# Performance work log

Measured on AMD Instinct MI355X. Metric: run time of the kernel, lower is better.

## Reference

```python
import jax, jax.numpy as jnp
import numpy as np

LOG2 = float(np.log(2.0))


def setup_inputs() -> dict:
    key = jax.random.key(0)
    ks = jax.random.split(key, 10)
    V, G, F, T = 262144, 4096, 256, 2
    node_feats = jax.random.normal(ks[0], (V, F), dtype=jnp.float32)
    segment_ids = jnp.sort(jax.random.randint(ks[1], (V,), 0, G))
    s = 0.05
    return {
        "node_feats": node_feats,
        "segment_ids": segment_ids,
        "num_graphs": G,
        "logit_w": jax.random.normal(ks[2], (T, 2 * F, 1), dtype=jnp.float32) * s,
        "logit_b": jnp.zeros((T, 1), dtype=jnp.float32),
        "proj_w": jax.random.normal(ks[3], (T, F, F), dtype=jnp.float32) * s,
        "proj_b": jnp.zeros((T, F), dtype=jnp.float32),
        "gru_w_ih": jax.random.normal(ks[4], (T, 3 * F, F), dtype=jnp.float32) * s,
        "gru_w_hh": jax.random.normal(ks[5], (T, 3 * F, F), dtype=jnp.float32) * s,
        "gru_b_ih": jnp.zeros((T, 3 * F), dtype=jnp.float32),
        "gru_b_hh": jnp.zeros((T, 3 * F), dtype=jnp.float32),
    }


def _gru_cell(x, h, w_ih, w_hh, b_ih, b_hh):
    # torch.nn.GRUCell math
    gi = x @ w_ih.T + b_ih  # [G, 3F]
    gh = h @ w_hh.T + b_hh
    i_r, i_z, i_n = jnp.split(gi, 3, axis=-1)
    h_r, h_z, h_n = jnp.split(gh, 3, axis=-1)
    r = jax.nn.sigmoid(i_r + h_r)
    z = jax.nn.sigmoid(i_z + h_z)
    n = jnp.tanh(i_n + r * h_n)
    return (1.0 - z) * n + z * h


def reference(node_feats, segment_ids, num_graphs, logit_w, logit_b,
              proj_w, proj_b, gru_w_ih, gru_w_hh, gru_b_ih, gru_b_hh):
    G = int(num_graphs)
    # initial graph feats: sum of node feats per graph
    g_feats = jax.ops.segment_sum(node_feats, segment_ids, num_segments=G)
    T = logit_w.shape[0]
    for t in range(T):
        # broadcast relu(g_feats) to nodes, concat with node feats, compute logits
        ctx_nodes = jax.nn.relu(g_feats)[segment_ids]              # [V, F]
        z = jnp.concatenate([ctx_nodes, node_feats], axis=-1) @ logit_w[t] + logit_b[t]  # [V,1]
        z = jnp.logaddexp(z, 0.0) - LOG2                           # SoftPlus2
        # segment softmax over nodes within each graph
        zmax = jax.ops.segment_max(z, segment_ids, num_segments=G)
        e = jnp.exp(z - zmax[segment_ids])
        denom = jax.ops.segment_sum(e, segment_ids, num_segments=G)
        a = e / denom[segment_ids]                                 # [V,1]
        # project nodes (dropout=0) and attention-weighted sum per graph
        hv = node_feats @ proj_w[t] + proj_b[t]                    # [V, F]
        g_repr = jax.ops.segment_sum(a * hv, segment_ids, num_segments=G)
        context = jax.nn.elu(g_repr)
        g_feats = _gru_cell(context, g_feats, gru_w_ih[t], gru_w_hh[t], gru_b_ih[t], gru_b_hh[t])
    return g_feats
```

## Files before the change

### kernel.cpp

```cpp
#include <hip/hip_runtime.h>
#include <hip/hip_bf16.h>
#include <math.h>

#define V_NODES 262144
#define NGRAPH  4096
#define FD      256
#define TSTEPS  2
#define GP      16
#define SB      1024
#define RS      264
#define EWCAP   2560

typedef unsigned short u16;
typedef __attribute__((ext_vector_type(8))) short short8;
typedef __attribute__((ext_vector_type(4))) float f32x4;

__device__ __forceinline__ float bf2f(u16 u) {
  union { unsigned int i; float f; } x; x.i = ((unsigned int)u) << 16; return x.f;
}
__device__ __forceinline__ u16 f2bf(float f) {
  union { unsigned int i; float f; } x; x.f = f;
  unsigned int r = x.i + 0x7FFFu + ((x.i >> 16) & 1u);
  return (u16)(r >> 16);
}
__device__ __forceinline__ unsigned int pkbf(float a, float b) {
  return (unsigned int)f2bf(a) | ((unsigned int)f2bf(b) << 16);
}
__device__ __forceinline__ float softplus2(float x) {
  return fmaxf(x, 0.0f) + log1pf(__expf(-fabsf(x))) - 0.69314718056f;
}
__device__ __forceinline__ float dot8(const float4 x0, const float4 x1, const float* w) {
  float d = fmaf(x0.x, w[0], fmaf(x0.y, w[1], fmaf(x0.z, w[2], x0.w * w[3])));
  return fmaf(x1.x, w[4], fmaf(x1.y, w[5], fmaf(x1.z, w[6], fmaf(x1.w, w[7], d))));
}

__global__ __launch_bounds__(256) void k_prep(
    const int* __restrict__ seg, const float* __restrict__ w_ih,
    const float* __restrict__ w_hh, const float* __restrict__ proj_w,
    int* __restrict__ start, u16* __restrict__ wihbf, u16* __restrict__ whhbf,
    u16* __restrict__ whhlo, u16* __restrict__ pwtbf) {
  __shared__ float tl[32][33];
  const int b = blockIdx.x, tid = threadIdx.x;
  const int gtid = b * 256 + tid;
  {
    const int v = gtid;
    const int s = seg[v];
    if (v == 0) {
      for (int g = 0; g <= s; ++g) start[g] = 0;
    } else {
      const int p = seg[v - 1];
      for (int g = p + 1; g <= s; ++g) start[g] = v;
    }
    if (v == V_NODES - 1)
      for (int g = s + 1; g <= NGRAPH; ++g) start[g] = V_NODES;
  }
  {
    const int nchunk = TSTEPS * 768 * FD / 4;
    if (gtid < nchunk) {
      const float4 x = ((const float4*)w_ih)[gtid];
      uint2 u; u.x = pkbf(x.x, x.y); u.y = pkbf(x.z, x.w);
      ((uint2*)wihbf)[gtid] = u;
      const float4 y = ((const float4*)w_hh)[gtid];
      const u16 h0 = f2bf(y.x), h1 = f2bf(y.y), h2 = f2bf(y.z), h3 = f2bf(y.w);
      uint2 hi_, lo_;
      hi_.x = (unsigned)h0 | ((unsigned)h1 << 16);
      hi_.y = (unsigned)h2 | ((unsigned)h3 << 16);
      lo_.x = pkbf(y.x - bf2f(h0), y.y - bf2f(h1));
      lo_.y = pkbf(y.z - bf2f(h2), y.w - bf2f(h3));
      ((uint2*)whhbf)[gtid] = hi_;
      ((uint2*)whhlo)[gtid] = lo_;
    }
  }
  if (b < 2 * 64) {
    const int t = b >> 6, tile = b & 63, bx = tile & 7, by = tile >> 3;
    const int tx = tid & 31, ty = tid >> 5;
    const float* S = proj_w + (size_t)t * FD * FD;
    u16* D = pwtbf + (size_t)t * FD * FD;
#pragma unroll
    for (int i = 0; i < 32; i += 8)
      tl[ty + i][tx] = S[(size_t)(by * 32 + ty + i) * FD + bx * 32 + tx];
    __syncthreads();
#pragma unroll
    for (int i = 0; i < 32; i += 8)
      D[(size_t)(bx * 32 + ty + i) * FD + by * 32 + tx] = f2bf(tl[tx][ty + i]);
  }
}

__global__ __launch_bounds__(256) void k_pass1(
    const float* __restrict__ nf, const int* __restrict__ start,
    const float* __restrict__ logit_w, float* __restrict__ gf,
    u16* __restrict__ nbf, float* __restrict__ d0, float* __restrict__ d1) {
  __shared__ __align__(16) float redf[8][FD];
  const int g = blockIdx.x, tid = threadIdx.x;
  const int h = tid >> 5, sl = tid & 31;
  const int s = start[g], e = start[g + 1];
  float wA[8], wB[8];
  {
    const float4 a0 = ((const float4*)(logit_w + FD))[2 * sl];
    const float4 a1 = ((const float4*)(logit_w + FD))[2 * sl + 1];
    const float4 b0 = ((const float4*)(logit_w + 512 + FD))[2 * sl];
    const float4 b1 = ((const float4*)(logit_w + 512 + FD))[2 * sl + 1];
    wA[0]=a0.x; wA[1]=a0.y; wA[2]=a0.z; wA[3]=a0.w;
    wA[4]=a1.x; wA[5]=a1.y; wA[6]=a1.z; wA[7]=a1.w;
    wB[0]=b0.x; wB[1]=b0.y; wB[2]=b0.z; wB[3]=b0.w;
    wB[4]=b1.x; wB[5]=b1.y; wB[6]=b1.z; wB[7]=b1.w;
  }
  float ac[8];
#pragma unroll
  for (int j = 0; j < 8; ++j) ac[j] = 0.f;
  const float4* nfv = (const float4*)nf;
  int v = s + h;
  for (; v + 24 < e; v += 32) {
    float4 x0[4], x1[4];
#pragma unroll
    for (int r = 0; r < 4; ++r) {
      x0[r] = nfv[(size_t)(v + 8 * r) * 64 + 2 * sl];
      x1[r] = nfv[(size_t)(v + 8 * r) * 64 + 2 * sl + 1];
    }
#pragma unroll
    for (int r = 0; r < 4; ++r) {
      uint4 u;
      u.x = pkbf(x0[r].x, x0[r].y); u.y = pkbf(x0[r].z, x0[r].w);
      u.z = pkbf(x1[r].x, x1[r].y); u.w = pkbf(x1[r].z, x1[r].w);
      ((uint4*)(nbf + (size_t)(v + 8 * r) * FD))[sl] = u;
      ac[0] += x0[r].x; ac[1] += x0[r].y; ac[2] += x0[r].z; ac[3] += x0[r].w;
      ac[4] += x1[r].x; ac[5] += x1[r].y; ac[6] += x1[r].z; ac[7] += x1[r].w;
    }
    float dA[4], dB[4];
#pragma unroll
    for (int r = 0; r < 4; ++r) {
      dA[r] = dot8(x0[r], x1[r], wA);
      dB[r] = dot8(x0[r], x1[r], wB);
    }
#pragma unroll
    for (int off = 1; off < 32; off <<= 1) {
#pragma unroll
      for (int r = 0; r < 4; ++r) {
        dA[r] += __shfl_xor(dA[r], off, 64);
        dB[r] += __shfl_xor(dB[r], off, 64);
      }
    }
    if (sl == 0) {
#pragma unroll
      for (int r = 0; r < 4; ++r) { d0[v + 8 * r] = dA[r]; d1[v + 8 * r] = dB[r]; }
    }
  }
  for (; v < e; v += 8) {
    const float4 x0 = nfv[(size_t)v * 64 + 2 * sl];
    const float4 x1 = nfv[(size_t)v * 64 + 2 * sl + 1];
    uint4 u0;
    u0.x = pkbf(x0.x, x0.y); u0.y = pkbf(x0.z, x0.w);
    u0.z = pkbf(x1.x, x1.y); u0.w = pkbf(x1.z, x1.w);
    ((uint4*)(nbf + (size_t)v * FD))[sl] = u0;
    ac[0] += x0.x; ac[1] += x0.y; ac[2] += x0.z; ac[3] += x0.w;
    ac[4] += x1.x; ac[5] += x1.y; ac[6] += x1.z; ac[7] += x1.w;
    float dA0 = dot8(x0, x1, wA), dB0 = dot8(x0, x1, wB);
#pragma unroll
    for (int off = 1; off < 32; off <<= 1) {
      dA0 += __shfl_xor(dA0, off, 64); dB0 += __shfl_xor(dB0, off, 64);
    }
    if (sl == 0) { d0[v] = dA0; d1[v] = dB0; }
  }
  ((float4*)&redf[h][sl * 8])[0] = make_float4(ac[0], ac[1], ac[2], ac[3]);
  ((float4*)&redf[h][sl * 8])[1] = make_float4(ac[4], ac[5], ac[6], ac[7]);
  __syncthreads();
  float sum = 0.f;
#pragma unroll
  for (int j = 0; j < 8; ++j) sum += redf[j][tid];
  gf[(size_t)g * FD + tid] = sum;
}

__global__ __launch_bounds__(SB, 4) void k_steps(
    const int* __restrict__ start, const float* __restrict__ logit_w,
    const float* __restrict__ logit_b, const float* __restrict__ proj_b,
    const float* __restrict__ b_ih, const float* __restrict__ b_hh,
    const u16* __restrict__ nbf, const float* __restrict__ d0,
    const float* __restrict__ d1, float* __restrict__ gf_out,
    const u16* __restrict__ wihbf, const u16* __restrict__ whhbf,
    const u16* __restrict__ whhlo, const u16* __restrict__ pwtbf) {
  __shared__ __align__(16) float gf_s[GP][FD];
  __shared__ __align__(16) float ew[EWCAP];
  __shared__ __align__(16) u16 wns_s[GP * RS];
  __shared__ __align__(16) u16 ctx_s[GP * RS];
  __shared__ __align__(16) u16 hhi_s[GP * RS];
  __shared__ __align__(16) u16 hlo_s[GP * RS];

  const int b = blockIdx.x, tid = threadIdx.x;
  const int wv = tid >> 6, lane = tid & 63;
  const int half = lane >> 5, sl = lane & 31;
  const int g0 = b * GP;
  const int g = g0 + wv;
  const int vs = start[g0];
  const int s = start[g], e = start[g + 1];

  ((float4*)gf_s)[tid] = ((const float4*)(gf_out + (size_t)g0 * FD))[tid];
  __syncthreads();

  for (int t = 0; t < TSTEPS; ++t) {
    for (int i = tid; i < GP * FD; i += SB) {
      const float x = gf_s[i >> 8][i & 255];
      const u16 hb = f2bf(x);
      hhi_s[(i >> 8) * RS + (i & 255)] = hb;
      hlo_s[(i >> 8) * RS + (i & 255)] = f2bf(x - bf2f(hb));
    }
    {
      const float lb = logit_b[t];
      const float* dt = t ? d1 : d0;
      const float4 h4 = ((const float4*)&gf_s[wv][0])[lane];
      const float4 w4 = ((const float4*)(logit_w + (size_t)t * 512))[lane];
      float c = fmaf(fmaxf(h4.x, 0.f), w4.x, fmaf(fmaxf(h4.y, 0.f), w4.y,
                fmaf(fmaxf(h4.z, 0.f), w4.z, fmaxf(h4.w, 0.f) * w4.w)));
#pragma unroll
      for (int off = 1; off < 64; off <<= 1) c += __shfl_xor(c, off, 64);
      float m = -1e30f;
      for (int v2 = s + lane; v2 < e; v2 += 64) {
        const float z = softplus2(c + dt[v2] + lb);
        ew[v2 - vs] = z;
        m = fmaxf(m, z);
      }
#pragma unroll
      for (int off = 1; off < 64; off <<= 1) m = fmaxf(m, __shfl_xor(m, off, 64));
      float ls = 0.f;
      for (int v2 = s + lane; v2 < e; v2 += 64) {
        const float ez = __expf(ew[v2 - vs] - m);
        ew[v2 - vs] = ez;
        ls += ez;
      }
#pragma unroll
      for (int off = 1; off < 64; off <<= 1) ls += __shfl_xor(ls, off, 64);
      const float inv = (e > s) ? 1.0f / ls : 0.f;
      for (int v2 = s + lane; v2 < e; v2 += 64) ew[v2 - vs] *= inv;
      float acc[8];
#pragma unroll
      for (int j = 0; j < 8; ++j) acc[j] = 0.f;
      int v = s + half;
      for (; v + 14 < e; v += 16) {
        uint4 u[8];
#pragma unroll
        for (int r = 0; r < 8; ++r)
          u[r] = ((const uint4*)(nbf + (size_t)(v + 2 * r) * FD))[sl];
#pragma unroll
        for (int r = 0; r < 8; ++r) {
          const float a = ew[v + 2 * r - vs];
          acc[0] = fmaf(a, bf2f((u16)(u[r].x & 0xffff)), acc[0]);
          acc[1] = fmaf(a, bf2f((u16)(u[r].x >> 16)),    acc[1]);
          acc[2] = fmaf(a, bf2f((u16)(u[r].y & 0xffff)), acc[2]);
          acc[3] = fmaf(a, bf2f((u16)(u[r].y >> 16)),    acc[3]);
          acc[4] = fmaf(a, bf2f((u16)(u[r].z & 0xffff)), acc[4]);
          acc[5] = fmaf(a, bf2f((u16)(u[r].z >> 16)),    acc[5]);
          acc[6] = fmaf(a, bf2f((u16)(u[r].w & 0xffff)), acc[6]);
          acc[7] = fmaf(a, bf2f((u16)(u[r].w >> 16)),    acc[7]);
        }
      }
      for (; v < e; v += 2) {
        const uint4 u0 = ((const uint4*)(nbf + (size_t)v * FD))[sl];
        const float a0 = ew[v - vs];
        acc[0] = fmaf(a0, bf2f((u16)(u0.x & 0xffff)), acc[0]);
        acc[1] = fmaf(a0, bf2f((u16)(u0.x >> 16)),    acc[1]);
        acc[2] = fmaf(a0, bf2f((u16)(u0.y & 0xffff)), acc[2]);
        acc[3] = fmaf(a0, bf2f((u16)(u0.y >> 16)),    acc[3]);
        acc[4] = fmaf(a0, bf2f((u16)(u0.z & 0xffff)), acc[4]);
        acc[5] = fmaf(a0, bf2f((u16)(u0.z >> 16)),    acc[5]);
        acc[6] = fmaf(a0, bf2f((u16)(u0.w & 0xffff)), acc[6]);
        acc[7] = fmaf(a0, bf2f((u16)(u0.w >> 16)),    acc[7]);
      }
#pragma unroll
      for (int j = 0; j < 8; ++j) acc[j] += __shfl_xor(acc[j], 32, 64);
      if (half == 0) {
        uint4 w;
        w.x = pkbf(acc[0], acc[1]); w.y = pkbf(acc[2], acc[3]);
        w.z = pkbf(acc[4], acc[5]); w.w = pkbf(acc[6], acc[7]);
        *(uint4*)(wns_s + wv * RS + sl * 8) = w;
      }
    }
    __syncthreads();
    {
      const int r = lane & 15, q = lane >> 4;
      const u16* xp = wns_s + r * RS + q * 8;
      const u16* wp = pwtbf + (size_t)t * FD * FD + (size_t)(wv * 16 + r) * FD + q * 8;
      f32x4 a4 = {0.f, 0.f, 0.f, 0.f};
#pragma unroll
      for (int kt = 0; kt < 8; ++kt) {
        const short8 av = *(const short8*)(xp + kt * 32);
        const short8 bv = *(const short8*)(wp + kt * 32);
        a4 = __builtin_amdgcn_mfma_f32_16x16x32_bf16(av, bv, a4, 0, 0, 0);
      }
      const int gcol = wv * 16 + r;
      const float bs = proj_b[t * FD + gcol];
#pragma unroll
      for (int i = 0; i < 4; ++i) {
        float vv = a4[i] + bs;
        vv = (vv > 0.0f) ? vv : expm1f(vv);
        ctx_s[(q * 4 + i) * RS + gcol] = f2bf(vv);
      }
    }
    __syncthreads();
    {
      const int r = lane & 15, q = lane >> 4;
      const u16* xi = ctx_s + r * RS + q * 8;
      const u16* xh = hhi_s + r * RS + q * 8;
      const u16* xl = hlo_s + r * RS + q * 8;
      const u16* wih_t = wihbf + (size_t)t * 768 * FD;
      const u16* whh_t = whhbf + (size_t)t * 768 * FD;
      const u16* whl_t = whhlo + (size_t)t * 768 * FD;
      auto gpair = [&](const u16* wi, const u16* wh, const u16* wl,
                       f32x4& ai, f32x4& ah) {
#pragma unroll
        for (int kt = 0; kt < 8; ++kt) {
          const short8 aiv = *(const short8*)(xi + kt * 32);
          const short8 bi  = *(const short8*)(wi + kt * 32);
          ai = __builtin_amdgcn_mfma_f32_16x16x32_bf16(aiv, bi, ai, 0, 0, 0);
          const short8 xhh = *(const short8*)(xh + kt * 32);
          const short8 xll = *(const short8*)(xl + kt * 32);
          const short8 bh  = *(const short8*)(wh + kt * 32);
          const short8 bl  = *(const short8*)(wl + kt * 32);
          ah = __builtin_amdgcn_mfma_f32_16x16x32_bf16(xhh, bh, ah, 0, 0, 0);
          ah = __builtin_amdgcn_mfma_f32_16x16x32_bf16(xll, bh, ah, 0, 0, 0);
          ah = __builtin_amdgcn_mfma_f32_16x16x32_bf16(xhh, bl, ah, 0, 0, 0);
        }
      };
      const int col = wv * 16 + r;
      float rr[4], zz[4];
      {
        f32x4 ai = {0.f,0.f,0.f,0.f}, ah = {0.f,0.f,0.f,0.f};
        gpair(wih_t + (size_t)col * FD + q * 8,
              whh_t + (size_t)col * FD + q * 8,
              whl_t + (size_t)col * FD + q * 8, ai, ah);
        const float bi_ = b_ih[t * 768 + col], bh_ = b_hh[t * 768 + col];
#pragma unroll
        for (int i = 0; i < 4; ++i)
          rr[i] = 1.f / (1.f + __expf(-(ai[i] + bi_ + ah[i] + bh_)));
      }
      {
        f32x4 ai = {0.f,0.f,0.f,0.f}, ah = {0.f,0.f,0.f,0.f};
        gpair(wih_t + (size_t)(256 + col) * FD + q * 8,
              whh_t + (size_t)(256 + col) * FD + q * 8,
              whl_t + (size_t)(256 + col) * FD + q * 8, ai, ah);
        const float bi_ = b_ih[t * 768 + 256 + col], bh_ = b_hh[t * 768 + 256 + col];
#pragma unroll
        for (int i = 0; i < 4; ++i)
          zz[i] = 1.f / (1.f + __expf(-(ai[i] + bi_ + ah[i] + bh_)));
      }
      {
        f32x4 ai = {0.f,0.f,0.f,0.f}, ah = {0.f,0.f,0.f,0.f};
        gpair(wih_t + (size_t)(512 + col) * FD + q * 8,
              whh_t + (size_t)(512 + col) * FD + q * 8,
              whl_t + (size_t)(512 + col) * FD + q * 8, ai, ah);
        const float bi_ = b_ih[t * 768 + 512 + col], bh_ = b_hh[t * 768 + 512 + col];
#pragma unroll
        for (int i = 0; i < 4; ++i) {
          const int row = q * 4 + i;
          const float nn = tanhf(ai[i] + bi_ + rr[i] * (ah[i] + bh_));
          const float hold = gf_s[row][col];
          gf_s[row][col] = (1.f - zz[i]) * nn + zz[i] * hold;
        }
      }
    }
    __syncthreads();
  }

  ((float4*)(gf_out + (size_t)g0 * FD))[tid] = ((const float4*)gf_s)[tid];
}

extern "C" void kernel_launch(void* const* d_in, const int* in_sizes, int n_in,
                              void* d_out, int out_size, void* d_ws, size_t ws_size,
                              hipStream_t stream) {
  const float* node    = (const float*)d_in[0];
  const int*   seg     = (const int*)d_in[1];
  const float* logit_w = (const float*)d_in[3];
  const float* logit_b = (const float*)d_in[4];
  const float* proj_w  = (const float*)d_in[5];
  const float* proj_b  = (const float*)d_in[6];
  const float* w_ih    = (const float*)d_in[7];
  const float* w_hh    = (const float*)d_in[8];
  const float* b_ih    = (const float*)d_in[9];
  const float* b_hh    = (const float*)d_in[10];
  float* gfeats = (float*)d_out;

  char* p = (char*)d_ws;
  int* start   = (int*)p;   p += (((NGRAPH + 1) * sizeof(int)) + 255) & ~(size_t)255;
  u16* nbf     = (u16*)p;   p += (size_t)V_NODES * FD * 2;
  float* d0    = (float*)p; p += (size_t)V_NODES * 4;
  float* d1    = (float*)p; p += (size_t)V_NODES * 4;
  u16* wihbf   = (u16*)p;   p += (size_t)TSTEPS * 768 * FD * 2;
  u16* whhbf   = (u16*)p;   p += (size_t)TSTEPS * 768 * FD * 2;
  u16* whhlo   = (u16*)p;   p += (size_t)TSTEPS * 768 * FD * 2;
  u16* pwtbf   = (u16*)p;   p += (size_t)TSTEPS * FD * FD * 2;
  (void)ws_size; (void)in_sizes; (void)n_in; (void)out_size;

  k_prep<<<dim3(V_NODES / 256), dim3(256), 0, stream>>>(
      seg, w_ih, w_hh, proj_w, start, wihbf, whhbf, whhlo, pwtbf);
  k_pass1<<<dim3(NGRAPH), dim3(256), 0, stream>>>(
      node, start, logit_w, gfeats, nbf, d0, d1);
  k_steps<<<dim3(NGRAPH / GP), dim3(SB), 0, stream>>>(
      start, logit_w, logit_b, proj_b, b_ih, b_hh, nbf, d0, d1,
      gfeats, wihbf, whhbf, whhlo, pwtbf);
}
```

Baseline: 537.1 us.

## Map one wavefront per graph in pass1 and write GRU output directly

k_pass1 now assigns a whole 64-lane wavefront to each graph (four graphs per block). Each lane owns four features and processes eight nodes per iteration. This removes the shared-memory reduction and __syncthreads used to combine per-half-wave partial sums. In k_steps, the last timestep writes GRU results straight to global memory, dropping the final barrier and the copy-out from shared memory. The trade-off is a single wavefront per graph with a 6-level shuffle reduction per node dot product, plus a stray redundant d0 store for lanes < 8.

```diff
diff --git a/kernel.cpp b/kernel.cpp
--- a/kernel.cpp
+++ b/kernel.cpp
@@ -29,9 +29,8 @@
 __device__ __forceinline__ float softplus2(float x) {
   return fmaxf(x, 0.0f) + log1pf(__expf(-fabsf(x))) - 0.69314718056f;
 }
-__device__ __forceinline__ float dot8(const float4 x0, const float4 x1, const float* w) {
-  float d = fmaf(x0.x, w[0], fmaf(x0.y, w[1], fmaf(x0.z, w[2], x0.w * w[3])));
-  return fmaf(x1.x, w[4], fmaf(x1.y, w[5], fmaf(x1.z, w[6], fmaf(x1.w, w[7], d))));
+__device__ __forceinline__ float dot4(const float4 x, const float4 w) {
+  return fmaf(x.x, w.x, fmaf(x.y, w.y, fmaf(x.z, w.z, x.w * w.w)));
 }
 
 __global__ __launch_bounds__(256) void k_prep(
@@ -90,84 +89,54 @@
     const float* __restrict__ nf, const int* __restrict__ start,
     const float* __restrict__ logit_w, float* __restrict__ gf,
     u16* __restrict__ nbf, float* __restrict__ d0, float* __restrict__ d1) {
-  __shared__ __align__(16) float redf[8][FD];
-  const int g = blockIdx.x, tid = threadIdx.x;
-  const int h = tid >> 5, sl = tid & 31;
+  const int wv = threadIdx.x >> 6, lane = threadIdx.x & 63;
+  const int g = blockIdx.x * 4 + wv;
   const int s = start[g], e = start[g + 1];
-  float wA[8], wB[8];
-  {
-    const float4 a0 = ((const float4*)(logit_w + FD))[2 * sl];
-    const float4 a1 = ((const float4*)(logit_w + FD))[2 * sl + 1];
-    const float4 b0 = ((const float4*)(logit_w + 512 + FD))[2 * sl];
-    const float4 b1 = ((const float4*)(logit_w + 512 + FD))[2 * sl + 1];
-    wA[0]=a0.x; wA[1]=a0.y; wA[2]=a0.z; wA[3]=a0.w;
-    wA[4]=a1.x; wA[5]=a1.y; wA[6]=a1.z; wA[7]=a1.w;
-    wB[0]=b0.x; wB[1]=b0.y; wB[2]=b0.z; wB[3]=b0.w;
-    wB[4]=b1.x; wB[5]=b1.y; wB[6]=b1.z; wB[7]=b1.w;
-  }
-  float ac[8];
-#pragma unroll
-  for (int j = 0; j < 8; ++j) ac[j] = 0.f;
+  const float4 wA = ((const float4*)(logit_w + FD))[lane];
+  const float4 wB = ((const float4*)(logit_w + 512 + FD))[lane];
+  float4 ac = make_float4(0.f, 0.f, 0.f, 0.f);
   const float4* nfv = (const float4*)nf;
-  int v = s + h;
-  for (; v + 24 < e; v += 32) {
-    float4 x0[4], x1[4];
-#pragma unroll
-    for (int r = 0; r < 4; ++r) {
-      x0[r] = nfv[(size_t)(v + 8 * r) * 64 + 2 * sl];
-      x1[r] = nfv[(size_t)(v + 8 * r) * 64 + 2 * sl + 1];
-    }
-#pragma unroll
-    for (int r = 0; r < 4; ++r) {
-      uint4 u;
-      u.x = pkbf(x0[r].x, x0[r].y); u.y = pkbf(x0[r].z, x0[r].w);
-      u.z = pkbf(x1[r].x, x1[r].y); u.w = pkbf(x1[r].z, x1[r].w);
-      ((uint4*)(nbf + (size_t)(v + 8 * r) * FD))[sl] = u;
-      ac[0] += x0[r].x; ac[1] += x0[r].y; ac[2] += x0[r].z; ac[3] += x0[r].w;
-      ac[4] += x1[r].x; ac[5] += x1[r].y; ac[6] += x1[r].z; ac[7] += x1[r].w;
-    }
-    float dA[4], dB[4];
-#pragma unroll
-    for (int r = 0; r < 4; ++r) {
-      dA[r] = dot8(x0[r], x1[r], wA);
-      dB[r] = dot8(x0[r], x1[r], wB);
-    }
-#pragma unroll
-    for (int off = 1; off < 32; off <<= 1) {
-#pragma unroll
-      for (int r = 0; r < 4; ++r) {
+  int v = s;
+  for (; v + 7 < e; v += 8) {
+    float4 x[8];
+#pragma unroll
+    for (int r = 0; r < 8; ++r) x[r] = nfv[(size_t)(v + r) * 64 + lane];
+#pragma unroll
+    for (int r = 0; r < 8; ++r) {
+      uint2 u; u.x = pkbf(x[r].x, x[r].y); u.y = pkbf(x[r].z, x[r].w);
+      ((uint2*)(nbf + (size_t)(v + r) * FD))[lane] = u;
+      ac.x += x[r].x; ac.y += x[r].y; ac.z += x[r].z; ac.w += x[r].w;
+    }
+    float dA[8], dB[8];
+#pragma unroll
+    for (int r = 0; r < 8; ++r) { dA[r] = dot4(x[r], wA); dB[r] = dot4(x[r], wB); }
+#pragma unroll
+    for (int off = 1; off < 64; off <<= 1) {
+#pragma unroll
+      for (int r = 0; r < 8; ++r) {
         dA[r] += __shfl_xor(dA[r], off, 64);
         dB[r] += __shfl_xor(dB[r], off, 64);
       }
     }
-    if (sl == 0) {
-#pragma unroll
-      for (int r = 0; r < 4; ++r) { d0[v + 8 * r] = dA[r]; d1[v + 8 * r] = dB[r]; }
-    }
-  }
-  for (; v < e; v += 8) {
-    const float4 x0 = nfv[(size_t)v * 64 + 2 * sl];
-    const float4 x1 = nfv[(size_t)v * 64 + 2 * sl + 1];
-    uint4 u0;
-    u0.x = pkbf(x0.x, x0.y); u0.y = pkbf(x0.z, x0.w);
-    u0.z = pkbf(x1.x, x1.y); u0.w = pkbf(x1.z, x1.w);
-    ((uint4*)(nbf + (size_t)v * FD))[sl] = u0;
-    ac[0] += x0.x; ac[1] += x0.y; ac[2] += x0.z; ac[3] += x0.w;
-    ac[4] += x1.x; ac[5] += x1.y; ac[6] += x1.z; ac[7] += x1.w;
-    float dA0 = dot8(x0, x1, wA), dB0 = dot8(x0, x1, wB);
-#pragma unroll
-    for (int off = 1; off < 32; off <<= 1) {
-      dA0 += __shfl_xor(dA0, off, 64); dB0 += __shfl_xor(dB0, off, 64);
-    }
-    if (sl == 0) { d0[v] = dA0; d1[v] = dB0; }
-  }
-  ((float4*)&redf[h][sl * 8])[0] = make_float4(ac[0], ac[1], ac[2], ac[3]);
-  ((float4*)&redf[h][sl * 8])[1] = make_float4(ac[4], ac[5], ac[6], ac[7]);
-  __syncthreads();
-  float sum = 0.f;
-#pragma unroll
-  for (int j = 0; j < 8; ++j) sum += redf[j][tid];
-  gf[(size_t)g * FD + tid] = sum;
+    if (lane < 8) d0[v + lane] = dA[0], d0[v + lane] = dA[lane];
+    if (lane == 0) {
+#pragma unroll
+      for (int r = 0; r < 8; ++r) { d0[v + r] = dA[r]; d1[v + r] = dB[r]; }
+    }
+  }
+  for (; v < e; ++v) {
+    const float4 x = nfv[(size_t)v * 64 + lane];
+    uint2 u; u.x = pkbf(x.x, x.y); u.y = pkbf(x.z, x.w);
+    ((uint2*)(nbf + (size_t)v * FD))[lane] = u;
+    ac.x += x.x; ac.y += x.y; ac.z += x.z; ac.w += x.w;
+    float dA = dot4(x, wA), dB = dot4(x, wB);
+#pragma unroll
+    for (int off = 1; off < 64; off <<= 1) {
+      dA += __shfl_xor(dA, off, 64); dB += __shfl_xor(dB, off, 64);
+    }
+    if (lane == 0) { d0[v] = dA; d1[v] = dB; }
+  }
+  ((float4*)(gf + (size_t)g * FD))[lane] = ac;
 }
 
 __global__ __launch_bounds__(SB, 4) void k_steps(
@@ -196,6 +165,7 @@
   ((float4*)gf_s)[tid] = ((const float4*)(gf_out + (size_t)g0 * FD))[tid];
   __syncthreads();
 
+#pragma unroll
   for (int t = 0; t < TSTEPS; ++t) {
     for (int i = tid; i < GP * FD; i += SB) {
       const float x = gf_s[i >> 8][i & 255];
@@ -351,15 +321,17 @@
         for (int i = 0; i < 4; ++i) {
           const int row = q * 4 + i;
           const float nn = tanhf(ai[i] + bi_ + rr[i] * (ah[i] + bh_));
-          const float hold = gf_s[row][col];
-          gf_s[row][col] = (1.f - zz[i]) * nn + zz[i] * hold;
+          const float hnew = (1.f - zz[i]) * nn + zz[i] * gf_s[row][col];
+          if (t == TSTEPS - 1) {
+            gf_out[(size_t)(g0 + row) * FD + col] = hnew;
+          } else {
+            gf_s[row][col] = hnew;
+          }
         }
       }
     }
-    __syncthreads();
-  }
-
-  ((float4*)(gf_out + (size_t)g0 * FD))[tid] = ((const float4*)gf_s)[tid];
+    if (t != TSTEPS - 1) __syncthreads();
+  }
 }
 
 extern "C" void kernel_launch(void* const* d_in, const int* in_sizes, int n_in,
@@ -390,7 +362,7 @@
 
   k_prep<<<dim3(V_NODES / 256), dim3(256), 0, stream>>>(
       seg, w_ih, w_hh, proj_w, start, wihbf, whhbf, whhlo, pwtbf);
-  k_pass1<<<dim3(NGRAPH), dim3(256), 0, stream>>>(
+  k_pass1<<<dim3(NGRAPH / 4), dim3(256), 0, stream>>>(
       node, start, logit_w, gfeats, nbf, d0, d1);
   k_steps<<<dim3(NGRAPH / GP), dim3(SB), 0, stream>>>(
       start, logit_w, logit_b, proj_b, b_ih, b_hh, nbf, d0, d1,
```

New measurement: 546.7 us. No clear change (+1.8%).
